# Optimization experiments

Hardware: AMD Instinct MI355X
Metric: run time of the kernel (lower is better)

The kernel has to match this reference:

```python
import jax, jax.numpy as jnp
import numpy as np

D_MODEL = 1024
NUM_HEADS = 16
HEAD_DIM = D_MODEL // NUM_HEADS


def setup_inputs() -> dict:
    key = jax.random.key(0)
    ks = jax.random.split(key, 11)
    B, S = 2, 2048
    scale = 1.0 / np.sqrt(D_MODEL)
    inp = {
        "q": jax.random.normal(ks[0], (B, S, D_MODEL), jnp.float32),
        "k": jax.random.normal(ks[1], (B, S, D_MODEL), jnp.float32),
        "v": jax.random.normal(ks[2], (B, S, D_MODEL), jnp.float32),
        "Wq": jax.random.normal(ks[3], (D_MODEL, D_MODEL), jnp.float32) * scale,
        "bq": jnp.zeros((D_MODEL,), jnp.float32),
        "Wk": jax.random.normal(ks[4], (D_MODEL, D_MODEL), jnp.float32) * scale,
        "bk": jnp.zeros((D_MODEL,), jnp.float32),
        "Wv": jax.random.normal(ks[5], (D_MODEL, D_MODEL), jnp.float32) * scale,
        "bv": jnp.zeros((D_MODEL,), jnp.float32),
        "Wo": jax.random.normal(ks[6], (D_MODEL, D_MODEL), jnp.float32) * scale,
        "bo": jnp.zeros((D_MODEL,), jnp.float32),
    }
    return inp


def reference(q, k, v, Wq, bq, Wk, bk, Wv, bv, Wo, bo):
    B, S, _ = q.shape
    # Linear projections (torch Linear: x @ W.T + b), split into heads -> [b,h,s,d]
    def proj(x, W, b):
        y = jnp.einsum('bsm,nm->bsn', x, W) + b
        return y.reshape(B, -1, NUM_HEADS, HEAD_DIM).transpose(0, 2, 1, 3)
    qh = proj(q, Wq, bq)
    kh = proj(k, Wk, bk)
    vh = proj(v, Wv, bv)
    # NOTE: source scales by sqrt(d_model), NOT sqrt(head_dim) -- faithful quirk
    factor = jnp.sqrt(jnp.float32(D_MODEL))
    scores = jnp.einsum('bhqd,bhkd->bhqk', qh, kh) / factor
    attn = jax.nn.softmax(scores, axis=-1)
    out = jnp.einsum('bhqk,bhkd->bhqd', attn, vh)
    out = out.transpose(0, 2, 1, 3).reshape(B, S, D_MODEL)
    # out projection; dropout=0.0 (eval) is identity
    return jnp.einsum('bsm,nm->bsn', out, Wo) + bo
```

## Files before the change

### kernel.cpp

```cpp
#include <hip/hip_runtime.h>
#include <hip/hip_bf16.h>

typedef __hip_bfloat16 bf16;
typedef short short8 __attribute__((ext_vector_type(8)));
typedef short bs4 __attribute__((ext_vector_type(4)));
typedef float f32x4 __attribute__((ext_vector_type(4)));

#define MFMA_BF16(a, b, c) __builtin_amdgcn_mfma_f32_16x16x32_bf16(a, b, c, 0, 0, 0)
#define MFMA16_BF16(a, b, c) __builtin_amdgcn_mfma_f32_16x16x16bf16_1k(a, b, c, 0, 0, 0)

#define QSCALE 0.045084439f

__device__ __forceinline__ void async_copy16(const bf16* g, bf16* l) {
    __builtin_amdgcn_global_load_lds(
        (const __attribute__((address_space(1))) unsigned int*)(const void*)g,
        (__attribute__((address_space(3))) unsigned int*)(void*)l, 16, 0, 0);
}

__global__ __launch_bounds__(256) void convert_all(
    const float* __restrict__ q, const float* __restrict__ k, const float* __restrict__ v,
    const float* __restrict__ wq, const float* __restrict__ wk,
    const float* __restrict__ wv, const float* __restrict__ wo,
    bf16* __restrict__ qb, bf16* __restrict__ kb, bf16* __restrict__ vb,
    bf16* __restrict__ wqb, bf16* __restrict__ wkb, bf16* __restrict__ wvb,
    bf16* __restrict__ wob)
{
    int blk = blockIdx.x;
    const float* s; bf16* d; int rel;
    if      (blk < 1024) { s = q;  d = qb;  rel = blk; }
    else if (blk < 2048) { s = k;  d = kb;  rel = blk - 1024; }
    else if (blk < 3072) { s = v;  d = vb;  rel = blk - 2048; }
    else if (blk < 3328) { s = wq; d = wqb; rel = blk - 3072; }
    else if (blk < 3584) { s = wk; d = wkb; rel = blk - 3328; }
    else if (blk < 3840) { s = wv; d = wvb; rel = blk - 3584; }
    else                 { s = wo; d = wob; rel = blk - 3840; }
    size_t base = (size_t)rel * 1024 + threadIdx.x;
#pragma unroll
    for (int i = 0; i < 4; i++) {
        float4 f = ((const float4*)s)[base + i * 256];
        union { bf16 h[4]; uint2 u; } pk;
        pk.h[0] = (bf16)f.x; pk.h[1] = (bf16)f.y;
        pk.h[2] = (bf16)f.z; pk.h[3] = (bf16)f.w;
        ((uint2*)d)[base + i * 256] = pk.u;
    }
}

__global__ __launch_bounds__(256) void gemm_qkv(
    const bf16* __restrict__ qb, const bf16* __restrict__ kb, const bf16* __restrict__ vb,
    const bf16* __restrict__ wqb, const bf16* __restrict__ wkb, const bf16* __restrict__ wvb,
    const float* __restrict__ bq, const float* __restrict__ bk, const float* __restrict__ bv,
    bf16* __restrict__ Qp, bf16* __restrict__ Kp, bf16* __restrict__ Vt)
{
    __shared__ bf16 Al[128 * 64];
    __shared__ bf16 Bl[128 * 64];

    const int sel = blockIdx.y >> 3;
    const bf16* A; const bf16* W; const float* bias;
    if      (sel == 0) { A = qb; W = wqb; bias = bq; }
    else if (sel == 1) { A = kb; W = wkb; bias = bk; }
    else               { A = vb; W = wvb; bias = bv; }

    const int K = 1024, N = 1024;
    const int t = threadIdx.x;
    const int lane = t & 63, wave = t >> 6;
    const int ln = lane & 15, quad = lane >> 4;
    const int wm = wave >> 1, wn = wave & 1;
    const int m0 = blockIdx.x * 128, n0 = (blockIdx.y & 7) * 128;

    f32x4 acc[4][4];
#pragma unroll
    for (int i = 0; i < 4; i++)
#pragma unroll
        for (int j = 0; j < 4; j++) acc[i][j] = (f32x4){0.f, 0.f, 0.f, 0.f};

    const int lk = ln & 7;
    const int srow = t >> 3, sidx0 = t & 7;

    for (int k0 = 0; k0 < K; k0 += 64) {
        const bf16* Ab = A + (size_t)m0 * K + k0;
        const bf16* Wb = W + (size_t)n0 * K + k0;
#pragma unroll
        for (int p = 0; p < 4; p++) {
            int row = p * 32 + srow, idx = sidx0 ^ (row & 7);
            async_copy16(Ab + (size_t)row * K + idx * 8, &Al[(p * 256 + wave * 64) * 8]);
        }
#pragma unroll
        for (int p = 0; p < 4; p++) {
            int row = p * 32 + srow, idx = sidx0 ^ (row & 7);
            async_copy16(Wb + (size_t)row * K + idx * 8, &Bl[(p * 256 + wave * 64) * 8]);
        }
        __syncthreads();

#pragma unroll
        for (int kk = 0; kk < 2; kk++) {
            short8 af[4], bfr[4];
#pragma unroll
            for (int i = 0; i < 4; i++) {
                int r = wm * 64 + i * 16 + ln;
                af[i] = *(const short8*)&Al[r * 64 + (((kk << 2) | quad) ^ lk) * 8];
            }
#pragma unroll
            for (int j = 0; j < 4; j++) {
                int r = wn * 64 + j * 16 + ln;
                bfr[j] = *(const short8*)&Bl[r * 64 + (((kk << 2) | quad) ^ lk) * 8];
            }
#pragma unroll
            for (int i = 0; i < 4; i++)
#pragma unroll
                for (int j = 0; j < 4; j++)
                    acc[i][j] = MFMA_BF16(af[i], bfr[j], acc[i][j]);
        }
        __syncthreads();
    }

#pragma unroll
    for (int j = 0; j < 4; j++) {
        int c = n0 + wn * 64 + j * 16 + ln;
        float bv2 = bias[c];
        if (sel == 2) {
            int h = c >> 6, dd = c & 63;
#pragma unroll
            for (int i = 0; i < 4; i++) {
                int m = m0 + wm * 64 + i * 16 + quad * 4;
                int bb = m >> 11, s = m & 2047;
                union { bf16 h4[4]; uint2 u; } pk;
#pragma unroll
                for (int r = 0; r < 4; r++) pk.h4[r] = (bf16)(acc[i][j][r] + bv2);
                *(uint2*)&Vt[(((size_t)(bb * 16 + h)) * 64 + dd) * 2048 + s] = pk.u;
            }
        } else {
            bf16* out = (sel == 0) ? Qp : Kp;
            float scl = (sel == 0) ? QSCALE : 1.0f;
#pragma unroll
            for (int i = 0; i < 4; i++) {
                int rb = m0 + wm * 64 + i * 16 + quad * 4;
#pragma unroll
                for (int r = 0; r < 4; r++)
                    out[(size_t)(rb + r) * N + c] = (bf16)((acc[i][j][r] + bv2) * scl);
            }
        }
    }
}

__global__ __launch_bounds__(256) void gemm_fin(
    const bf16* __restrict__ A, const bf16* __restrict__ W,
    const float* __restrict__ bias, float* __restrict__ C)
{
    __shared__ bf16 Al[128 * 64];
    __shared__ bf16 Bl[64 * 64];

    const int K = 1024, N = 1024;
    const int t = threadIdx.x;
    const int lane = t & 63, wave = t >> 6;
    const int ln = lane & 15, quad = lane >> 4;
    const int wm = wave >> 1, wn = wave & 1;
    const int m0 = blockIdx.x * 128, n0 = blockIdx.y * 64;

    f32x4 acc[4][2];
#pragma unroll
    for (int i = 0; i < 4; i++)
#pragma unroll
        for (int j = 0; j < 2; j++) acc[i][j] = (f32x4){0.f, 0.f, 0.f, 0.f};

    const int lk = ln & 7;
    const int srow = t >> 3, sidx0 = t & 7;

    for (int k0 = 0; k0 < K; k0 += 64) {
        const bf16* Ab = A + (size_t)m0 * K + k0;
        const bf16* Wb = W + (size_t)n0 * K + k0;
#pragma unroll
        for (int p = 0; p < 4; p++) {
            int row = p * 32 + srow, idx = sidx0 ^ (row & 7);
            async_copy16(Ab + (size_t)row * K + idx * 8, &Al[(p * 256 + wave * 64) * 8]);
        }
#pragma unroll
        for (int p = 0; p < 2; p++) {
            int row = p * 32 + srow, idx = sidx0 ^ (row & 7);
            async_copy16(Wb + (size_t)row * K + idx * 8, &Bl[(p * 256 + wave * 64) * 8]);
        }
        __syncthreads();

#pragma unroll
        for (int kk = 0; kk < 2; kk++) {
            short8 af[4], bfr[2];
#pragma unroll
            for (int i = 0; i < 4; i++) {
                int r = wm * 64 + i * 16 + ln;
                af[i] = *(const short8*)&Al[r * 64 + (((kk << 2) | quad) ^ lk) * 8];
            }
#pragma unroll
            for (int j = 0; j < 2; j++) {
                int r = wn * 32 + j * 16 + ln;
                bfr[j] = *(const short8*)&Bl[r * 64 + (((kk << 2) | quad) ^ lk) * 8];
            }
#pragma unroll
            for (int i = 0; i < 4; i++)
#pragma unroll
                for (int j = 0; j < 2; j++)
                    acc[i][j] = MFMA_BF16(af[i], bfr[j], acc[i][j]);
        }
        __syncthreads();
    }

#pragma unroll
    for (int j = 0; j < 2; j++) {
        int c = n0 + wn * 32 + j * 16 + ln;
        float bv2 = bias[c];
#pragma unroll
        for (int i = 0; i < 4; i++) {
            int rb = m0 + wm * 64 + i * 16 + quad * 4;
#pragma unroll
            for (int r = 0; r < 4; r++)
                C[(size_t)(rb + r) * N + c] = acc[i][j][r] + bv2;
        }
    }
}

__global__ __launch_bounds__(512) void attn128q(
    const bf16* __restrict__ Q, const bf16* __restrict__ K,
    const bf16* __restrict__ V, bf16* __restrict__ O)
{
    const int S = 2048, D = 1024;
    __shared__ bf16 Kl[2][128 * 64];
    __shared__ bf16 Vl[2][64 * 128];

    const int t = threadIdx.x, lane = t & 63, wave = t >> 6;
    const int ln = lane & 15, quad = lane >> 4;
    const int h = blockIdx.x & 15, b = blockIdx.x >> 4, qt = blockIdx.y;
    const size_t kqbase = (size_t)b * S * D + (size_t)h * 64;
    const size_t vbase = ((size_t)(b * 16 + h)) * 64 * 2048;

    short8 aq0, aq1;
    {
        const bf16* qp = Q + kqbase + (size_t)(qt * 128 + wave * 16 + ln) * D;
        aq0 = *(const short8*)(qp + quad * 8);
        aq1 = *(const short8*)(qp + 32 + quad * 8);
    }
    asm volatile("" :: "v"(aq0), "v"(aq1));

    f32x4 o[4];
    f32x4 l4 = (f32x4){0.f, 0.f, 0.f, 0.f};
#pragma unroll
    for (int i = 0; i < 4; i++) o[i] = (f32x4){0.f, 0.f, 0.f, 0.f};

    const int lk = ln & 7;
    const int kof0 = ln * 64 + ((quad ^ lk) * 8);
    const int kof1 = ln * 64 + (((4 | quad) ^ lk) * 8);
    int vof[8];
#pragma unroll
    for (int nk = 0; nk < 8; nk++)
        vof[nk] = ln * 128 + (((nk * 2 + (quad >> 1)) ^ lk) * 8 + (quad & 1) * 4);

    const int krow = t >> 3, kidx = t & 7;
    const int vrow = t >> 4, vidx = t & 15;

#define STAGE_KV(buf_, kt_) do {                                               \
    _Pragma("unroll")                                                          \
    for (int p = 0; p < 2; p++) {                                              \
        int row = p * 64 + krow, idx = kidx ^ (row & 7);                       \
        async_copy16(K + kqbase + (size_t)((kt_) * 128 + row) * D + idx * 8,   \
                     &Kl[buf_][(p * 512 + wave * 64) * 8]);                    \
    }                                                                          \
    _Pragma("unroll")                                                          \
    for (int p = 0; p < 2; p++) {                                              \
        int row = p * 32 + vrow, idx = vidx ^ (row & 7);                       \
        async_copy16(V + vbase + (size_t)row * 2048 + (kt_) * 128 + idx * 8,   \
                     &Vl[buf_][(p * 512 + wave * 64) * 8]);                    \
    }                                                                          \
} while (0)

    STAGE_KV(0, 0);

    for (int kt = 0; kt < S / 128; kt++) {
        const int cur = kt & 1;
        if (kt < S / 128 - 1) {
            STAGE_KV(cur ^ 1, kt + 1);
            asm volatile("s_waitcnt vmcnt(4)" ::: "memory");
        } else {
            asm volatile("s_waitcnt vmcnt(0)" ::: "memory");
        }
        __builtin_amdgcn_s_barrier();

        const bf16* Klc = Kl[cur];
        const bf16* Vlc = Vl[cur];

#pragma unroll
        for (int nk = 0; nk < 8; nk++) {
            short8 kf0 = *(const short8*)&Klc[nk * 1024 + kof0];
            short8 kf1 = *(const short8*)&Klc[nk * 1024 + kof1];

            __builtin_amdgcn_s_setprio(1);
            f32x4 a = (f32x4){0.f, 0.f, 0.f, 0.f};
            a = MFMA_BF16(kf0, aq0, a);
            a = MFMA_BF16(kf1, aq1, a);
            __builtin_amdgcn_s_setprio(0);

            bs4 pa;
            {
                union { bs4 s4; bf16 hh[4]; } pk;
                f32x4 p;
#pragma unroll
                for (int r = 0; r < 4; r++) {
                    p[r] = __builtin_amdgcn_exp2f(a[r]);
                    pk.hh[r] = (bf16)p[r];
                }
                l4 += p;
                pa = pk.s4;
            }

            __builtin_amdgcn_s_setprio(1);
#pragma unroll
            for (int nd = 0; nd < 4; nd++) {
                bs4 vb = *(const bs4*)&Vlc[nd * 2048 + vof[nk]];
                o[nd] = MFMA16_BF16(pa, vb, o[nd]);
            }
            __builtin_amdgcn_s_setprio(0);
        }

        asm volatile("" ::: "memory");
        __builtin_amdgcn_s_barrier();
    }
#undef STAGE_KV

    {
        float lv = (l4[0] + l4[1]) + (l4[2] + l4[3]);
        lv += __shfl_xor(lv, 16);
        lv += __shfl_xor(lv, 32);
#pragma unroll
        for (int r = 0; r < 4; r++) {
            float inv = __builtin_amdgcn_rcpf(__shfl(lv, quad * 4 + r));
            int row = qt * 128 + wave * 16 + quad * 4 + r;
#pragma unroll
            for (int nd = 0; nd < 4; nd++)
                O[((size_t)b * S + row) * D + h * 64 + nd * 16 + ln] =
                    (bf16)(o[nd][r] * inv);
        }
    }
}

extern "C" void kernel_launch(void* const* d_in, const int* in_sizes, int n_in,
                              void* d_out, int out_size, void* d_ws, size_t ws_size,
                              hipStream_t stream) {
    (void)in_sizes; (void)n_in; (void)out_size; (void)ws_size;
    const float* q  = (const float*)d_in[0];
    const float* k  = (const float*)d_in[1];
    const float* v  = (const float*)d_in[2];
    const float* Wq = (const float*)d_in[3];
    const float* bq = (const float*)d_in[4];
    const float* Wk = (const float*)d_in[5];
    const float* bk = (const float*)d_in[6];
    const float* Wv = (const float*)d_in[7];
    const float* bv = (const float*)d_in[8];
    const float* Wo = (const float*)d_in[9];
    const float* bo = (const float*)d_in[10];
    float* out = (float*)d_out;

    const int M = 4096, N = 1024;
    const size_t MN = (size_t)M * N;
    const size_t NN = (size_t)N * N;
    bf16* qb  = (bf16*)d_ws;
    bf16* kb  = qb + MN;
    bf16* vb  = kb + MN;
    bf16* wqb = vb + MN;
    bf16* wkb = wqb + NN;
    bf16* wvb = wkb + NN;
    bf16* wob = wvb + NN;
    bf16* Qp  = wob + NN;
    bf16* Kp  = Qp + MN;
    bf16* Vt  = Kp + MN;
    bf16* AO  = qb;

    dim3 blk(256);
    convert_all<<<4096, blk, 0, stream>>>(q, k, v, Wq, Wk, Wv, Wo,
                                          qb, kb, vb, wqb, wkb, wvb, wob);

    gemm_qkv<<<dim3(32, 24), blk, 0, stream>>>(qb, kb, vb, wqb, wkb, wvb,
                                               bq, bk, bv, Qp, Kp, Vt);

    attn128q<<<dim3(32, 16), dim3(512), 0, stream>>>(Qp, Kp, Vt, AO);

    gemm_fin<<<dim3(32, 16), blk, 0, stream>>>(AO, wob, bo, out);
}
```

Measured before the change: 221.4 us.

## Switch attention to 32x32 MFMA with key-split waves and LDS reduction

Rewrites the attention inner loop to use 32x32x16 bf16 MFMA instructions. Each wave now owns 32 query rows and half of the keys in every 128-key tile, instead of 16 query rows over all keys. The two key-half partial outputs and row sums are combined through LDS at the end. The V swizzle is widened to match the new fragment reads, and launch bounds now request 4 blocks per SM. The aim is fewer, larger MFMA issues and fewer LDS fragment loads per FLOP, at the cost of more accumulator registers and an extra reduction step.

```diff
diff --git a/kernel.cpp b/kernel.cpp
--- a/kernel.cpp
+++ b/kernel.cpp
@@ -5,9 +5,10 @@
 typedef short short8 __attribute__((ext_vector_type(8)));
 typedef short bs4 __attribute__((ext_vector_type(4)));
 typedef float f32x4 __attribute__((ext_vector_type(4)));
+typedef float f32x16 __attribute__((ext_vector_type(16)));
 
 #define MFMA_BF16(a, b, c) __builtin_amdgcn_mfma_f32_16x16x32_bf16(a, b, c, 0, 0, 0)
-#define MFMA16_BF16(a, b, c) __builtin_amdgcn_mfma_f32_16x16x16bf16_1k(a, b, c, 0, 0, 0)
+#define MFMA32_BF16(a, b, c) __builtin_amdgcn_mfma_f32_32x32x16_bf16(a, b, c, 0, 0, 0)
 
 #define QSCALE 0.045084439f
 
@@ -216,7 +217,7 @@
     }
 }
 
-__global__ __launch_bounds__(512) void attn128q(
+__global__ __launch_bounds__(512, 4) void attn128q(
     const bf16* __restrict__ Q, const bf16* __restrict__ K,
     const bf16* __restrict__ V, bf16* __restrict__ O)
 {
@@ -225,31 +226,35 @@
     __shared__ bf16 Vl[2][64 * 128];
 
     const int t = threadIdx.x, lane = t & 63, wave = t >> 6;
-    const int ln = lane & 15, quad = lane >> 4;
+    const int lo = lane & 31, hi = lane >> 5;
+    const int keyhalf = wave >> 2;
+    const int qw = wave & 3;
     const int h = blockIdx.x & 15, b = blockIdx.x >> 4, qt = blockIdx.y;
     const size_t kqbase = (size_t)b * S * D + (size_t)h * 64;
     const size_t vbase = ((size_t)(b * 16 + h)) * 64 * 2048;
 
-    short8 aq0, aq1;
+    const int q0 = qt * 128 + qw * 32;
+    short8 aq[4];
     {
-        const bf16* qp = Q + kqbase + (size_t)(qt * 128 + wave * 16 + ln) * D;
-        aq0 = *(const short8*)(qp + quad * 8);
-        aq1 = *(const short8*)(qp + 32 + quad * 8);
-    }
-    asm volatile("" :: "v"(aq0), "v"(aq1));
-
-    f32x4 o[4];
+        const bf16* qp = Q + kqbase + (size_t)(q0 + lo) * D + hi * 8;
+#pragma unroll
+        for (int s = 0; s < 4; s++) aq[s] = *(const short8*)(qp + s * 16);
+    }
+    asm volatile("" :: "v"(aq[0]), "v"(aq[1]), "v"(aq[2]), "v"(aq[3]));
+
+    f32x16 o0, o1;
+#pragma unroll
+    for (int i = 0; i < 16; i++) { o0[i] = 0.f; o1[i] = 0.f; }
     f32x4 l4 = (f32x4){0.f, 0.f, 0.f, 0.f};
-#pragma unroll
-    for (int i = 0; i < 4; i++) o[i] = (f32x4){0.f, 0.f, 0.f, 0.f};
-
-    const int lk = ln & 7;
-    const int kof0 = ln * 64 + ((quad ^ lk) * 8);
-    const int kof1 = ln * 64 + (((4 | quad) ^ lk) * 8);
-    int vof[8];
-#pragma unroll
-    for (int nk = 0; nk < 8; nk++)
-        vof[nk] = ln * 128 + (((nk * 2 + (quad >> 1)) ^ lk) * 8 + (quad & 1) * 4);
+
+    int koff[4];
+#pragma unroll
+    for (int s = 0; s < 4; s++)
+        koff[s] = lo * 64 + (((2 * s + hi) ^ (lo & 7)) * 8);
+    const int khbase = keyhalf * 64 * 64;
+
+    const int x0 = (keyhalf * 8) ^ (lo & 15);
+    const int vbl = lo * 128 + hi * 4;
 
     const int krow = t >> 3, kidx = t & 7;
     const int vrow = t >> 4, vidx = t & 15;
@@ -263,7 +268,7 @@
     }                                                                          \
     _Pragma("unroll")                                                          \
     for (int p = 0; p < 2; p++) {                                              \
-        int row = p * 32 + vrow, idx = vidx ^ (row & 7);                       \
+        int row = p * 32 + vrow, idx = vidx ^ (row & 15);                      \
         async_copy16(V + vbase + (size_t)row * 2048 + (kt_) * 128 + idx * 8,   \
                      &Vl[buf_][(p * 512 + wave * 64) * 8]);                    \
     }                                                                          \
@@ -285,34 +290,49 @@
         const bf16* Vlc = Vl[cur];
 
 #pragma unroll
-        for (int nk = 0; nk < 8; nk++) {
-            short8 kf0 = *(const short8*)&Klc[nk * 1024 + kof0];
-            short8 kf1 = *(const short8*)&Klc[nk * 1024 + kof1];
+        for (int kg = 0; kg < 2; kg++) {
+            const bf16* kb = Klc + khbase + kg * (32 * 64);
+            short8 kf0 = *(const short8*)(kb + koff[0]);
+            short8 kf1 = *(const short8*)(kb + koff[1]);
+            short8 kf2 = *(const short8*)(kb + koff[2]);
+            short8 kf3 = *(const short8*)(kb + koff[3]);
 
             __builtin_amdgcn_s_setprio(1);
-            f32x4 a = (f32x4){0.f, 0.f, 0.f, 0.f};
-            a = MFMA_BF16(kf0, aq0, a);
-            a = MFMA_BF16(kf1, aq1, a);
+            f32x16 acc;
+#pragma unroll
+            for (int i = 0; i < 16; i++) acc[i] = 0.f;
+            acc = MFMA32_BF16(kf0, aq[0], acc);
+            acc = MFMA32_BF16(kf1, aq[1], acc);
+            acc = MFMA32_BF16(kf2, aq[2], acc);
+            acc = MFMA32_BF16(kf3, aq[3], acc);
             __builtin_amdgcn_s_setprio(0);
 
-            bs4 pa;
-            {
-                union { bs4 s4; bf16 hh[4]; } pk;
-                f32x4 p;
-#pragma unroll
-                for (int r = 0; r < 4; r++) {
-                    p[r] = __builtin_amdgcn_exp2f(a[r]);
-                    pk.hh[r] = (bf16)p[r];
+            union { bf16 hh[8]; short8 s; } pk0, pk1;
+#pragma unroll
+            for (int r = 0; r < 8; r++) {
+                float p = __builtin_amdgcn_exp2f(acc[r]);
+                l4[r & 3] += p;
+                pk0.hh[r] = (bf16)p;
+            }
+#pragma unroll
+            for (int r = 0; r < 8; r++) {
+                float p = __builtin_amdgcn_exp2f(acc[8 + r]);
+                l4[r & 3] += p;
+                pk1.hh[r] = (bf16)p;
+            }
+
+            __builtin_amdgcn_s_setprio(1);
+#pragma unroll
+            for (int db = 0; db < 2; db++) {
+#pragma unroll
+                for (int c = 0; c < 2; c++) {
+                    const int m = kg * 4 + 2 * c;
+                    union { bs4 hh[2]; short8 s; } vf;
+                    vf.hh[0] = *(const bs4*)&Vlc[vbl + db * 4096 + ((x0 ^ m) * 8)];
+                    vf.hh[1] = *(const bs4*)&Vlc[vbl + db * 4096 + ((x0 ^ (m + 1)) * 8)];
+                    if (db == 0) o0 = MFMA32_BF16(c ? pk1.s : pk0.s, vf.s, o0);
+                    else         o1 = MFMA32_BF16(c ? pk1.s : pk0.s, vf.s, o1);
                 }
-                l4 += p;
-                pa = pk.s4;
-            }
-
-            __builtin_amdgcn_s_setprio(1);
-#pragma unroll
-            for (int nd = 0; nd < 4; nd++) {
-                bs4 vb = *(const bs4*)&Vlc[nd * 2048 + vof[nk]];
-                o[nd] = MFMA16_BF16(pa, vb, o[nd]);
             }
             __builtin_amdgcn_s_setprio(0);
         }
@@ -322,18 +342,35 @@
     }
 #undef STAGE_KV
 
-    {
-        float lv = (l4[0] + l4[1]) + (l4[2] + l4[3]);
-        lv += __shfl_xor(lv, 16);
-        lv += __shfl_xor(lv, 32);
-#pragma unroll
-        for (int r = 0; r < 4; r++) {
-            float inv = __builtin_amdgcn_rcpf(__shfl(lv, quad * 4 + r));
-            int row = qt * 128 + wave * 16 + quad * 4 + r;
-#pragma unroll
-            for (int nd = 0; nd < 4; nd++)
-                O[((size_t)b * S + row) * D + h * 64 + nd * 16 + ln] =
-                    (bf16)(o[nd][r] * inv);
+    float lv = (l4[0] + l4[1]) + (l4[2] + l4[3]);
+    lv += __shfl_xor(lv, 32);
+
+    float* os = (float*)&Kl[0][0];
+    float* ls = (float*)&Vl[0][0];
+    if (wave >= 4) {
+        const int w4 = wave - 4;
+#pragma unroll
+        for (int i = 0; i < 16; i++) os[(w4 * 32 + i) * 64 + lane] = o0[i];
+#pragma unroll
+        for (int i = 0; i < 16; i++) os[(w4 * 32 + 16 + i) * 64 + lane] = o1[i];
+        ls[w4 * 64 + lane] = lv;
+    }
+    __syncthreads();
+    if (wave < 4) {
+#pragma unroll
+        for (int i = 0; i < 16; i++) o0[i] += os[(wave * 32 + i) * 64 + lane];
+#pragma unroll
+        for (int i = 0; i < 16; i++) o1[i] += os[(wave * 32 + 16 + i) * 64 + lane];
+        lv += ls[wave * 64 + lane];
+        float inv = __builtin_amdgcn_rcpf(lv);
+#pragma unroll
+        for (int r = 0; r < 16; r++) {
+            const int q = (r & 3) + 8 * (r >> 2) + 4 * hi;
+            float invr = __shfl(inv, q);
+            const int row = qt * 128 + qw * 32 + q;
+            bf16* op = O + ((size_t)b * S + row) * D + h * 64 + lo;
+            op[0]  = (bf16)(o0[r] * invr);
+            op[32] = (bf16)(o1[r] * invr);
         }
     }
 }
```

Result: no change. 221.5 us (+0.0%).
